# Kernel tuning notes

Hardware: AMD Instinct MI355X
Metric: run time of the kernel (lower is better)

Reference implementation:

```python
import jax, jax.numpy as jnp
import numpy as np

EMBED_DIM = 512
NUM_HEADS = 16
TGT_LEN = 1024
BSZ = 4
HEAD_DIM = EMBED_DIM // NUM_HEADS


def setup_inputs() -> dict:
    key = jax.random.key(0)
    ks = jax.random.split(key, 12)
    E = EMBED_DIM
    s = 1.0 / np.sqrt(E)
    query = jax.random.normal(ks[0], (TGT_LEN, BSZ, E), dtype=jnp.float32)
    attn_bias = jax.random.normal(ks[1], (BSZ * NUM_HEADS, TGT_LEN, TGT_LEN), dtype=jnp.float32)
    key_padding_mask = jax.random.randint(ks[2], (BSZ, TGT_LEN), 0, 2) == 1
    q_w = jax.random.normal(ks[3], (E, E), dtype=jnp.float32) * s
    q_b = jax.random.normal(ks[4], (E,), dtype=jnp.float32) * 0.02
    k_w = jax.random.normal(ks[5], (E, E), dtype=jnp.float32) * s
    k_b = jax.random.normal(ks[6], (E,), dtype=jnp.float32) * 0.02
    v_w = jax.random.normal(ks[7], (E, E), dtype=jnp.float32) * s
    v_b = jax.random.normal(ks[8], (E,), dtype=jnp.float32) * 0.02
    out_w = jax.random.normal(ks[9], (E, E), dtype=jnp.float32) * s
    out_b = jax.random.normal(ks[10], (E,), dtype=jnp.float32) * 0.02
    return {
        "query": query, "attn_bias": attn_bias, "key_padding_mask": key_padding_mask,
        "q_w": q_w, "q_b": q_b, "k_w": k_w, "k_b": k_b,
        "v_w": v_w, "v_b": v_b, "out_w": out_w, "out_b": out_b,
    }


def reference(query, attn_bias, key_padding_mask, q_w, q_b, k_w, k_b, v_w, v_b, out_w, out_b):
    Tlen, B, E = query.shape
    H, hd = NUM_HEADS, HEAD_DIM
    scaling = hd ** -0.5
    # self-attention: q/k/v all from query (Linear uses y = x @ W.T + b)
    q = (query @ q_w.T + q_b) * scaling
    k = query @ k_w.T + k_b
    v = query @ v_w.T + v_b
    # [T, B, E] -> [B*H, T, hd]
    q = q.reshape(Tlen, B * H, hd).transpose(1, 0, 2)
    k = k.reshape(Tlen, B * H, hd).transpose(1, 0, 2)
    v = v.reshape(Tlen, B * H, hd).transpose(1, 0, 2)
    # scores [B*H, T, S]
    aw = jnp.einsum('bth,bsh->bts', q, k) + attn_bias
    # key padding mask: [B, S] -> broadcast over heads and tgt
    aw = aw.reshape(B, H, Tlen, Tlen)
    aw = jnp.where(key_padding_mask[:, None, None, :], -jnp.inf, aw)
    aw = aw.reshape(B * H, Tlen, Tlen)
    probs = jax.nn.softmax(aw.astype(jnp.float32), axis=-1)
    attn = jnp.einsum('bts,bsh->bth', probs.astype(query.dtype), v)
    attn = attn.transpose(1, 0, 2).reshape(Tlen, B, E)
    out = attn @ out_w.T + out_b
    # need_weights=True, need_head_weights=False -> mean over heads, [B, T, S]
    attn_weights_avg = probs.reshape(B, H, Tlen, Tlen).mean(axis=1)
    return out, attn_weights_avg
```

## Files before the change

### kernel.cpp

```cpp
#include <hip/hip_runtime.h>
#include <math.h>

typedef __bf16 bf16x8 __attribute__((ext_vector_type(8)));
typedef __bf16 bf16x4 __attribute__((ext_vector_type(4)));
typedef float  f32x4  __attribute__((ext_vector_type(4)));

#define WAIT_LGKM0() __builtin_amdgcn_s_waitcnt(0xC07F)

__global__ __launch_bounds__(256)
void cvt_w(const float* __restrict__ w0, const float* __restrict__ w1,
           const float* __restrict__ w2, const float* __restrict__ w3,
           __bf16* __restrict__ d0, __bf16* __restrict__ d1,
           __bf16* __restrict__ d2, __bf16* __restrict__ d3)
{
    const int y = blockIdx.y;
    const float* s = (y == 0) ? w0 : (y == 1) ? w1 : (y == 2) ? w2 : w3;
    __bf16*      d = (y == 0) ? d0 : (y == 1) ? d1 : (y == 2) ? d2 : d3;
    const int i = blockIdx.x * 256 + threadIdx.x;
    float4 a = *(const float4*)(s + (size_t)i * 8);
    float4 b = *(const float4*)(s + (size_t)i * 8 + 4);
    bf16x8 v;
    v[0] = (__bf16)a.x; v[1] = (__bf16)a.y; v[2] = (__bf16)a.z; v[3] = (__bf16)a.w;
    v[4] = (__bf16)b.x; v[5] = (__bf16)b.y; v[6] = (__bf16)b.z; v[7] = (__bf16)b.w;
    *(bf16x8*)(d + (size_t)i * 8) = v;
}

__global__ __launch_bounds__(256)
void qkv_proj(const float* __restrict__ X,
              const __bf16* __restrict__ Wqb, const __bf16* __restrict__ Wkb,
              const __bf16* __restrict__ Wvb,
              const float* __restrict__ bq, const float* __restrict__ bk,
              const float* __restrict__ bv,
              __bf16* __restrict__ qTb, __bf16* __restrict__ kTb,
              __bf16* __restrict__ vTb)
{
    const int z = blockIdx.z;
    const __bf16* Wb   = (z == 0) ? Wqb : (z == 1) ? Wkb : Wvb;
    const float*  bias = (z == 0) ? bq  : (z == 1) ? bk  : bv;

    const int tid  = threadIdx.x;
    const int w    = tid >> 6;
    const int lane = tid & 63;
    const int lq   = lane & 15;
    const int quad = lane >> 4;
    const int n0    = blockIdx.x * 64 + (w >> 1) * 32;
    const int obase = blockIdx.y * 128 + (w & 1) * 64;

    f32x4 acc[2][4] = {};
#pragma unroll 2
    for (int k0 = 0; k0 < 512; k0 += 32) {
        bf16x8 af[2], bfr[4];
#pragma unroll
        for (int m = 0; m < 2; m++) {
            const float* xp = X + (size_t)(n0 + m * 16 + lq) * 512 + k0 + quad * 8;
            float4 x0 = *(const float4*)xp;
            float4 x1 = *(const float4*)(xp + 4);
            bf16x8 v;
            v[0] = (__bf16)x0.x; v[1] = (__bf16)x0.y; v[2] = (__bf16)x0.z; v[3] = (__bf16)x0.w;
            v[4] = (__bf16)x1.x; v[5] = (__bf16)x1.y; v[6] = (__bf16)x1.z; v[7] = (__bf16)x1.w;
            af[m] = v;
        }
#pragma unroll
        for (int nn = 0; nn < 4; nn++)
            bfr[nn] = *(const bf16x8*)(Wb + (size_t)(obase + nn * 16 + lq) * 512 + k0 + quad * 8);
#pragma unroll
        for (int m = 0; m < 2; m++)
#pragma unroll
            for (int nn = 0; nn < 4; nn++)
                acc[m][nn] = __builtin_amdgcn_mfma_f32_16x16x32_bf16(af[m], bfr[nn], acc[m][nn], 0, 0, 0);
    }

    const float scaling = 0.17677669529663687f;
#pragma unroll
    for (int m = 0; m < 2; m++)
#pragma unroll
        for (int nn = 0; nn < 4; nn++)
#pragma unroll
            for (int r = 0; r < 4; r++) {
                const int n = n0 + m * 16 + quad * 4 + r;
                const int o = obase + nn * 16 + lq;
                float val = acc[m][nn][r] + bias[o];
                const int t = n >> 2, b = n & 3;
                const int h = o >> 5, d = o & 31;
                const int bh = b * 16 + h;
                if (z == 0)
                    qTb[(((size_t)bh * 1024 + t) << 5) + d] = (__bf16)(val * scaling);
                else if (z == 1)
                    kTb[(((size_t)bh * 1024 + t) << 5) + d] = (__bf16)val;
                else
                    vTb[(((size_t)bh * 32 + d) << 10) + t] = (__bf16)val;
            }
}

__global__ __launch_bounds__(256)
void out_proj(const __bf16* __restrict__ A, const __bf16* __restrict__ Wb,
              const float* __restrict__ bias, float* __restrict__ out)
{
    const int tid  = threadIdx.x;
    const int w    = tid >> 6;
    const int lane = tid & 63;
    const int lq   = lane & 15;
    const int quad = lane >> 4;
    const int n0    = blockIdx.x * 64 + (w >> 1) * 32;
    const int obase = blockIdx.y * 128 + (w & 1) * 64;

    f32x4 acc[2][4] = {};
#pragma unroll 2
    for (int k0 = 0; k0 < 512; k0 += 32) {
        bf16x8 af[2], bfr[4];
#pragma unroll
        for (int m = 0; m < 2; m++)
            af[m] = *(const bf16x8*)(A + (size_t)(n0 + m * 16 + lq) * 512 + k0 + quad * 8);
#pragma unroll
        for (int nn = 0; nn < 4; nn++)
            bfr[nn] = *(const bf16x8*)(Wb + (size_t)(obase + nn * 16 + lq) * 512 + k0 + quad * 8);
#pragma unroll
        for (int m = 0; m < 2; m++)
#pragma unroll
            for (int nn = 0; nn < 4; nn++)
                acc[m][nn] = __builtin_amdgcn_mfma_f32_16x16x32_bf16(af[m], bfr[nn], acc[m][nn], 0, 0, 0);
    }
#pragma unroll
    for (int m = 0; m < 2; m++)
#pragma unroll
        for (int nn = 0; nn < 4; nn++)
#pragma unroll
            for (int r = 0; r < 4; r++) {
                const int n = n0 + m * 16 + quad * 4 + r;
                const int o = obase + nn * 16 + lq;
                out[(size_t)n * 512 + o] = acc[m][nn][r] + bias[o];
            }
}

__global__ __launch_bounds__(512, 2)
void attn_mfma(const __bf16* __restrict__ qTb, const __bf16* __restrict__ kTb,
               const __bf16* __restrict__ vTb, const float* __restrict__ bias,
               const int* __restrict__ mask, __bf16* __restrict__ attnb,
               float* __restrict__ avgf)
{
    __shared__ float smem[17408];
    float* const Op0  = smem;
    float* const red0 = &smem[8448];
    __bf16* const Pbase = (__bf16*)&smem[8704];

    const int tid  = threadIdx.x;
    const int w    = tid >> 6;
    const int lane = tid & 63;
    const int lq   = lane & 15;
    const int quad = lane >> 4;

    const int bid = blockIdx.y * 64 + blockIdx.x;
    const int nb  = (bid & 7) * 32 + (bid >> 3);
    const int t0  = (nb & 63) * 16;
    const int b   = nb >> 6;
    const int sbase = w * 128;

    __bf16* const Pw = Pbase + w * 2176;

    unsigned mbits = 0;
    {
        const int* mp = mask + b * 1024 + sbase + quad * 4;
#pragma unroll
        for (int j = 0; j < 8; j++) {
            int4 m4 = *(const int4*)(mp + j * 16);
            mbits |= (unsigned)(m4.x != 0) << (j * 4 + 0);
            mbits |= (unsigned)(m4.y != 0) << (j * 4 + 1);
            mbits |= (unsigned)(m4.z != 0) << (j * 4 + 2);
            mbits |= (unsigned)(m4.w != 0) << (j * 4 + 3);
        }
    }

    const float* const bb = bias + (((size_t)(b * 16)) << 20) +
                            (((size_t)(t0 + lq)) << 10) + sbase + quad * 4;
    const __bf16* const qp0 = qTb + (((size_t)(b * 16) * 1024 + t0) << 5) +
                              lq * 32 + quad * 8;

    bf16x8 qa = *(const bf16x8*)qp0;
    f32x4 cj[8];
#pragma unroll
    for (int j = 0; j < 8; j++) cj[j] = *(const f32x4*)(bb + j * 16);

    float avg_reg[32] = {};

    for (int hh = 0; hh < 16; hh++) {
        const int bh = b * 16 + hh;
        float* const Op  = Op0  + (hh & 1) * 4224;
        float* const red = red0 + (hh & 1) * 128;
        const __bf16* kp = kTb + ((size_t)bh << 15);
        const __bf16* vp = vTb + ((size_t)bh << 15);

        bf16x8 kb[8];
#pragma unroll
        for (int j = 0; j < 8; j++)
            kb[j] = *(const bf16x8*)(kp + (size_t)(sbase + j * 16 + lq) * 32 + quad * 8);
        bf16x8 v0r[4], v1r[4];
#pragma unroll
        for (int ks = 0; ks < 4; ks++) {
            v0r[ks] = *(const bf16x8*)(vp + (size_t)lq * 1024 + sbase + ks * 32 + quad * 8);
            v1r[ks] = *(const bf16x8*)(vp + (size_t)(16 + lq) * 1024 + sbase + ks * 32 + quad * 8);
        }
        __builtin_amdgcn_sched_barrier(0);

        f32x4 acc[8];
        __builtin_amdgcn_s_setprio(1);
#pragma unroll
        for (int j = 0; j < 8; j++)
            acc[j] = __builtin_amdgcn_mfma_f32_16x16x32_bf16(kb[j], qa, cj[j], 0, 0, 0);
        __builtin_amdgcn_s_setprio(0);
        __builtin_amdgcn_sched_barrier(0);

        {
            const int hn = (hh + 1) & 15;
            qa = *(const bf16x8*)(qp0 + ((size_t)hn << 15));
            const float* bn = bb + ((size_t)hn << 20);
#pragma unroll
            for (int j = 0; j < 8; j++) cj[j] = *(const f32x4*)(bn + j * 16);
        }
        __builtin_amdgcn_sched_barrier(0);

        float sm = 0.f;
#pragma unroll
        for (int j = 0; j < 8; j++)
#pragma unroll
            for (int r = 0; r < 4; r++) {
                float p = __expf(acc[j][r]);
                p = ((mbits >> (j * 4 + r)) & 1u) ? 0.f : p;
                acc[j][r] = p;
                sm += p;
            }
        sm += __shfl_xor(sm, 16);
        sm += __shfl_xor(sm, 32);

#pragma unroll
        for (int j = 0; j < 8; j++) {
            bf16x4 pv;
            pv[0] = (__bf16)acc[j][0]; pv[1] = (__bf16)acc[j][1];
            pv[2] = (__bf16)acc[j][2]; pv[3] = (__bf16)acc[j][3];
            *(bf16x4*)&Pw[lq * 136 + j * 16 + quad * 4] = pv;
        }
        if (lane < 16) red[w * 16 + lane] = sm;

        f32x4 o0 = {0.f, 0.f, 0.f, 0.f}, o1 = {0.f, 0.f, 0.f, 0.f};
        __builtin_amdgcn_s_setprio(1);
#pragma unroll
        for (int ks = 0; ks < 4; ks++) {
            bf16x8 pa = *(const bf16x8*)&Pw[lq * 136 + ks * 32 + quad * 8];
            o0 = __builtin_amdgcn_mfma_f32_16x16x32_bf16(pa, v0r[ks], o0, 0, 0, 0);
            o1 = __builtin_amdgcn_mfma_f32_16x16x32_bf16(pa, v1r[ks], o1, 0, 0, 0);
        }
        __builtin_amdgcn_s_setprio(0);
#pragma unroll
        for (int r = 0; r < 4; r++) {
            Op[w * 528 + (quad * 4 + r) * 33 + lq]      = o0[r];
            Op[w * 528 + (quad * 4 + r) * 33 + 16 + lq] = o1[r];
        }

        __builtin_amdgcn_sched_barrier(0);
        asm volatile("" ::: "memory");
        WAIT_LGKM0();
        __builtin_amdgcn_s_barrier();
        asm volatile("" ::: "memory");
        __builtin_amdgcn_sched_barrier(0);

        {
            const int t = tid >> 5, d = tid & 31;
            float s = 0.f, o = 0.f;
#pragma unroll
            for (int w2 = 0; w2 < 8; w2++) s += red[w2 * 16 + t];
#pragma unroll
            for (int w2 = 0; w2 < 8; w2++) o += Op[w2 * 528 + t * 33 + d];
            attnb[((size_t)(t0 + t) * 4 + b) * 512 + hh * 32 + d] = (__bf16)(o / s);
        }

        float s_all = 0.f;
#pragma unroll
        for (int w2 = 0; w2 < 8; w2++) s_all += red[w2 * 16 + lq];
        const float inv = 1.0f / s_all;
#pragma unroll
        for (int j = 0; j < 8; j++)
#pragma unroll
            for (int r = 0; r < 4; r++)
                avg_reg[j * 4 + r] += acc[j][r] * inv;
    }

    float* ap = avgf + ((size_t)(b * 1024 + t0 + lq) << 10) + sbase + quad * 4;
#pragma unroll
    for (int j = 0; j < 8; j++) {
        f32x4 v = { avg_reg[j * 4 + 0] * 0.0625f, avg_reg[j * 4 + 1] * 0.0625f,
                    avg_reg[j * 4 + 2] * 0.0625f, avg_reg[j * 4 + 3] * 0.0625f };
        *(f32x4*)(ap + j * 16) = v;
    }
}

extern "C" void kernel_launch(void* const* d_in, const int* in_sizes, int n_in,
                              void* d_out, int out_size, void* d_ws, size_t ws_size,
                              hipStream_t stream)
{
    const float* query     = (const float*)d_in[0];
    const float* attn_bias = (const float*)d_in[1];
    const int*   mask      = (const int*)d_in[2];
    const float* q_w       = (const float*)d_in[3];
    const float* q_b       = (const float*)d_in[4];
    const float* k_w       = (const float*)d_in[5];
    const float* k_b       = (const float*)d_in[6];
    const float* v_w       = (const float*)d_in[7];
    const float* v_b       = (const float*)d_in[8];
    const float* out_w     = (const float*)d_in[9];
    const float* out_b     = (const float*)d_in[10];

    float* out     = (float*)d_out;
    float* avg_out = out + (size_t)2097152;

    char* wsb = (char*)d_ws;
    __bf16* Wqb   = (__bf16*)(wsb);
    __bf16* Wkb   = (__bf16*)(wsb + ((size_t)512 << 10));
    __bf16* Wvb   = (__bf16*)(wsb + ((size_t)1 << 20));
    __bf16* Wob   = (__bf16*)(wsb + ((size_t)1 << 20) + ((size_t)512 << 10));
    __bf16* qTb   = (__bf16*)(wsb + ((size_t)2  << 20));
    __bf16* kTb   = (__bf16*)(wsb + ((size_t)6  << 20));
    __bf16* vTb   = (__bf16*)(wsb + ((size_t)10 << 20));
    __bf16* attnb = (__bf16*)(wsb + ((size_t)14 << 20));

    cvt_w<<<dim3(128, 4), dim3(256), 0, stream>>>(
        q_w, k_w, v_w, out_w, Wqb, Wkb, Wvb, Wob);

    qkv_proj<<<dim3(64, 4, 3), dim3(256), 0, stream>>>(
        query, Wqb, Wkb, Wvb, q_b, k_b, v_b, qTb, kTb, vTb);

    attn_mfma<<<dim3(64, 4), dim3(512), 0, stream>>>(
        qTb, kTb, vTb, attn_bias, mask, attnb, avg_out);

    out_proj<<<dim3(64, 4), dim3(256), 0, stream>>>(attnb, Wob, out_b, out);
}
```

Measured before the change: 159.2 us.

## Split attention heads across two blocks and merge head-averaged weights in a follow-up kernel

The attention kernel grid gains a z dimension of 2, so each block handles 8 heads instead of 16, doubling the block count from 256 to 512 to fill more of the GPU's compute units. The z=0 half writes its partial head-average directly in fp32 and the z=1 half writes a bf16 partial to a workspace buffer. A new avg_add kernel then sums the two partials. This costs an extra launch, extra traffic over the 16M-element averaged output, and some precision loss from the bf16 partial.

```diff
diff --git a/kernel.cpp b/kernel.cpp
--- a/kernel.cpp
+++ b/kernel.cpp
@@ -136,7 +136,7 @@
 void attn_mfma(const __bf16* __restrict__ qTb, const __bf16* __restrict__ kTb,
                const __bf16* __restrict__ vTb, const float* __restrict__ bias,
                const int* __restrict__ mask, __bf16* __restrict__ attnb,
-               float* __restrict__ avgf)
+               float* __restrict__ avgf, __bf16* __restrict__ p1)
 {
     __shared__ float smem[17408];
     float* const Op0  = smem;
@@ -153,6 +153,7 @@
     const int nb  = (bid & 7) * 32 + (bid >> 3);
     const int t0  = (nb & 63) * 16;
     const int b   = nb >> 6;
+    const int z   = blockIdx.z;
     const int sbase = w * 128;
 
     __bf16* const Pw = Pbase + w * 2176;
@@ -170,10 +171,12 @@
         }
     }
 
-    const float* const bb = bias + (((size_t)(b * 16)) << 20) +
+    const float* const bb = bias + (((size_t)(b * 16 + z * 8)) << 20) +
                             (((size_t)(t0 + lq)) << 10) + sbase + quad * 4;
-    const __bf16* const qp0 = qTb + (((size_t)(b * 16) * 1024 + t0) << 5) +
+    const __bf16* const qp0 = qTb + (((size_t)((b * 16 + z * 8) * 1024 + t0)) << 5) +
                               lq * 32 + quad * 8;
+    const __bf16* const kp0 = kTb + ((size_t)(b * 16 + z * 8) << 15);
+    const __bf16* const vp0 = vTb + ((size_t)(b * 16 + z * 8) << 15);
 
     bf16x8 qa = *(const bf16x8*)qp0;
     f32x4 cj[8];
@@ -182,12 +185,11 @@
 
     float avg_reg[32] = {};
 
-    for (int hh = 0; hh < 16; hh++) {
-        const int bh = b * 16 + hh;
+    for (int hh = 0; hh < 8; hh++) {
         float* const Op  = Op0  + (hh & 1) * 4224;
         float* const red = red0 + (hh & 1) * 128;
-        const __bf16* kp = kTb + ((size_t)bh << 15);
-        const __bf16* vp = vTb + ((size_t)bh << 15);
+        const __bf16* kp = kp0 + ((size_t)hh << 15);
+        const __bf16* vp = vp0 + ((size_t)hh << 15);
 
         bf16x8 kb[8];
 #pragma unroll
@@ -210,7 +212,7 @@
         __builtin_amdgcn_sched_barrier(0);
 
         {
-            const int hn = (hh + 1) & 15;
+            const int hn = (hh + 1) & 7;
             qa = *(const bf16x8*)(qp0 + ((size_t)hn << 15));
             const float* bn = bb + ((size_t)hn << 20);
 #pragma unroll
@@ -269,7 +271,8 @@
             for (int w2 = 0; w2 < 8; w2++) s += red[w2 * 16 + t];
 #pragma unroll
             for (int w2 = 0; w2 < 8; w2++) o += Op[w2 * 528 + t * 33 + d];
-            attnb[((size_t)(t0 + t) * 4 + b) * 512 + hh * 32 + d] = (__bf16)(o / s);
+            attnb[((size_t)(t0 + t) * 4 + b) * 512 + (z * 8 + hh) * 32 + d] =
+                (__bf16)(o / s);
         }
 
         float s_all = 0.f;
@@ -283,13 +286,41 @@
                 avg_reg[j * 4 + r] += acc[j][r] * inv;
     }
 
-    float* ap = avgf + ((size_t)(b * 1024 + t0 + lq) << 10) + sbase + quad * 4;
-#pragma unroll
-    for (int j = 0; j < 8; j++) {
-        f32x4 v = { avg_reg[j * 4 + 0] * 0.0625f, avg_reg[j * 4 + 1] * 0.0625f,
-                    avg_reg[j * 4 + 2] * 0.0625f, avg_reg[j * 4 + 3] * 0.0625f };
-        *(f32x4*)(ap + j * 16) = v;
-    }
+    if (z == 0) {
+        float* ap = avgf + ((size_t)(b * 1024 + t0 + lq) << 10) + sbase + quad * 4;
+#pragma unroll
+        for (int j = 0; j < 8; j++) {
+            f32x4 v = { avg_reg[j * 4 + 0] * 0.0625f, avg_reg[j * 4 + 1] * 0.0625f,
+                        avg_reg[j * 4 + 2] * 0.0625f, avg_reg[j * 4 + 3] * 0.0625f };
+            *(f32x4*)(ap + j * 16) = v;
+        }
+    } else {
+        __bf16* pp = p1 + ((size_t)(b * 1024 + t0 + lq) << 10) + sbase + quad * 4;
+#pragma unroll
+        for (int j = 0; j < 8; j++) {
+            bf16x4 v;
+            v[0] = (__bf16)(avg_reg[j * 4 + 0] * 0.0625f);
+            v[1] = (__bf16)(avg_reg[j * 4 + 1] * 0.0625f);
+            v[2] = (__bf16)(avg_reg[j * 4 + 2] * 0.0625f);
+            v[3] = (__bf16)(avg_reg[j * 4 + 3] * 0.0625f);
+            *(bf16x4*)(pp + j * 16) = v;
+        }
+    }
+}
+
+__global__ __launch_bounds__(256)
+void avg_add(float* __restrict__ avg, const __bf16* __restrict__ p1)
+{
+    const size_t i = ((size_t)blockIdx.x * 256 + threadIdx.x) * 8;
+    bf16x8 a = *(const bf16x8*)(p1 + i);
+    float4 lo = *(float4*)(avg + i);
+    float4 hi = *(float4*)(avg + i + 4);
+    lo.x += (float)a[0]; lo.y += (float)a[1];
+    lo.z += (float)a[2]; lo.w += (float)a[3];
+    hi.x += (float)a[4]; hi.y += (float)a[5];
+    hi.z += (float)a[6]; hi.w += (float)a[7];
+    *(float4*)(avg + i)     = lo;
+    *(float4*)(avg + i + 4) = hi;
 }
 
 extern "C" void kernel_launch(void* const* d_in, const int* in_sizes, int n_in,
@@ -320,6 +351,7 @@
     __bf16* kTb   = (__bf16*)(wsb + ((size_t)6  << 20));
     __bf16* vTb   = (__bf16*)(wsb + ((size_t)10 << 20));
     __bf16* attnb = (__bf16*)(wsb + ((size_t)14 << 20));
+    __bf16* p1    = (__bf16*)(wsb + ((size_t)18 << 20));
 
     cvt_w<<<dim3(128, 4), dim3(256), 0, stream>>>(
         q_w, k_w, v_w, out_w, Wqb, Wkb, Wvb, Wob);
@@ -327,8 +359,10 @@
     qkv_proj<<<dim3(64, 4, 3), dim3(256), 0, stream>>>(
         query, Wqb, Wkb, Wvb, q_b, k_b, v_b, qTb, kTb, vTb);
 
-    attn_mfma<<<dim3(64, 4), dim3(512), 0, stream>>>(
-        qTb, kTb, vTb, attn_bias, mask, attnb, avg_out);
+    attn_mfma<<<dim3(64, 4, 2), dim3(512), 0, stream>>>(
+        qTb, kTb, vTb, attn_bias, mask, attnb, avg_out, p1);
+
+    avg_add<<<dim3(2048), dim3(256), 0, stream>>>(avg_out, p1);
 
     out_proj<<<dim3(64, 4), dim3(256), 0, stream>>>(attnb, Wob, out_b, out);
 }
```

Measured after the change: 171.4 us. 7.6% more time.
